# Optimization experiments

Hardware: AMD Instinct MI355X
Metric: run time of the kernel (lower is better)

Reference implementation:

```python
import jax, jax.numpy as jnp
import numpy as np

B, C, H, W = 8, 512, 32, 32
NUM_HEADS = 8
NUM_GROUPS = 32
EPS = 1e-5


def setup_inputs() -> dict:
    key = jax.random.key(0)
    k1, k2, k3 = jax.random.split(key, 3)
    x = jax.random.normal(k1, (B, C, H, W), dtype=jnp.float32)
    gn_w = jnp.ones((C,), dtype=jnp.float32)
    gn_b = jnp.zeros((C,), dtype=jnp.float32)
    qkv_w = jax.random.normal(k2, (3 * C, C), dtype=jnp.float32) * 0.02
    qkv_b = jnp.zeros((3 * C,), dtype=jnp.float32)
    # NOTE: original zero-initializes proj_out; we use random weights so the
    # residual branch is non-trivial for correctness testing.
    proj_w = jax.random.normal(k3, (C, C), dtype=jnp.float32) * 0.02
    proj_b = jnp.zeros((C,), dtype=jnp.float32)
    return {"x": x, "gn_w": gn_w, "gn_b": gn_b, "qkv_w": qkv_w,
            "qkv_b": qkv_b, "proj_w": proj_w, "proj_b": proj_b}


def _group_norm(x, w, b):
    # x: [B, C, T]
    Bn, Cn, T = x.shape
    xg = x.reshape(Bn, NUM_GROUPS, Cn // NUM_GROUPS, T)
    mean = xg.mean(axis=(2, 3), keepdims=True)
    var = xg.var(axis=(2, 3), keepdims=True)
    xn = ((xg - mean) * jax.lax.rsqrt(var + EPS)).reshape(Bn, Cn, T)
    return xn * w[None, :, None] + b[None, :, None]


def reference(x, gn_w, gn_b, qkv_w, qkv_b, proj_w, proj_b):
    b, c = x.shape[0], x.shape[1]
    spatial = x.shape[2:]
    xr = x.reshape(b, c, -1)                      # [B, C, T]
    xn = _group_norm(xr, gn_w, gn_b)
    # 1x1 conv1d: [3C, C] x [B, C, T] -> [B, 3C, T]
    qkv = jnp.einsum('oc,bct->bot', qkv_w, xn) + qkv_b[None, :, None]
    T = qkv.shape[-1]
    qkv = qkv.reshape(b * NUM_HEADS, -1, T)       # [B*Nh, 3*ch, T]
    ch = qkv.shape[1] // 3
    q, k, v = jnp.split(qkv, 3, axis=1)
    scale = 1.0 / np.sqrt(np.sqrt(ch))
    weight = jnp.einsum('bct,bcs->bts', q * scale, k * scale)  # [B*Nh, T, T]
    weight = jax.nn.softmax(weight.astype(jnp.float32), axis=-1).astype(weight.dtype)
    h = jnp.einsum('bts,bcs->bct', weight, v)     # [B*Nh, ch, T]
    h = h.reshape(b, c, T)
    h = jnp.einsum('oc,bct->bot', proj_w, h) + proj_b[None, :, None]
    return (xr + h).reshape(b, c, *spatial)
```

## Files before the change

### kernel.cpp

```cpp
#include <hip/hip_runtime.h>
#include <math.h>

#define Bn 8
#define Cn 512
#define Tn 1024

typedef __attribute__((ext_vector_type(8))) short bf16x8;
typedef __attribute__((ext_vector_type(4))) float f32x4;

__device__ __forceinline__ unsigned short f2bf(float f) {
  unsigned int u = __builtin_bit_cast(unsigned int, f);
  u = (u + 0x7FFFu + ((u >> 16) & 1u)) >> 16;
  return (unsigned short)u;
}

typedef __attribute__((address_space(1))) const unsigned int GU32;
typedef __attribute__((address_space(3))) unsigned int LU32;
__device__ __forceinline__ void gld16(const unsigned short* g, unsigned short* l) {
  __builtin_amdgcn_global_load_lds((GU32*)g, (LU32*)l, 16, 0, 0);
}

__device__ __forceinline__ void stage128x64(const unsigned short* __restrict__ src,
                                            size_t row_stride, unsigned short* lds, int tid) {
  const int w = tid >> 6;
  const int row = tid >> 3;
  const int sc = (tid & 7) ^ ((tid >> 3) & 7);
#pragma unroll
  for (int c = 0; c < 4; ++c)
    gld16(src + (size_t)(c * 32 + row) * row_stride + sc * 8,
          (unsigned short*)((char*)lds + c * 4096 + w * 1024));
}

__device__ __forceinline__ void stage64x64(const unsigned short* __restrict__ src,
                                           size_t row_stride, unsigned short* lds, int tid) {
  const int w = tid >> 6;
  const int row = tid >> 3;
  const int sc = (tid & 7) ^ ((tid >> 3) & 7);
#pragma unroll
  for (int c = 0; c < 2; ++c)
    gld16(src + (size_t)(c * 32 + row) * row_stride + sc * 8,
          (unsigned short*)((char*)lds + c * 4096 + w * 1024));
}

__global__ __launch_bounds__(256) void gn_kernel(const float* __restrict__ x,
                                                 const float* __restrict__ gw,
                                                 const float* __restrict__ gb,
                                                 unsigned short* __restrict__ xn_t) {
  const int blk = blockIdx.x;
  const int b = blk >> 5, g = blk & 31;
  const size_t base = ((size_t)b * Cn + (size_t)g * 16) * Tn;
  const float4* __restrict__ xin = (const float4*)(x + base);
  const int tid = threadIdx.x;

  float vv[16][4];
  float sum = 0.f, sq = 0.f;
#pragma unroll
  for (int k = 0; k < 16; ++k) {
    const float4 t4 = xin[tid + (k << 8)];
    vv[k][0] = t4.x; vv[k][1] = t4.y; vv[k][2] = t4.z; vv[k][3] = t4.w;
    sum += t4.x + t4.y + t4.z + t4.w;
    sq += t4.x * t4.x + t4.y * t4.y + t4.z * t4.z + t4.w * t4.w;
  }

  __shared__ float rs[8];
  const int lane = tid & 63, wv = tid >> 6;
#pragma unroll
  for (int off = 32; off > 0; off >>= 1) {
    sum += __shfl_down(sum, off);
    sq += __shfl_down(sq, off);
  }
  if (lane == 0) { rs[wv] = sum; rs[4 + wv] = sq; }
  __syncthreads();
  const float ts = rs[0] + rs[1] + rs[2] + rs[3];
  const float tq = rs[4] + rs[5] + rs[6] + rs[7];
  const float mean = ts * (1.f / 16384.f);
  const float var = tq * (1.f / 16384.f) - mean * mean;
  const float rstd = rsqrtf(var + 1e-5f);

  float aa[16], bb[16];
#pragma unroll
  for (int k = 0; k < 16; ++k) {
    aa[k] = rstd * gw[g * 16 + k];
    bb[k] = gb[g * 16 + k] - mean * aa[k];
  }

#pragma unroll
  for (int j = 0; j < 4; ++j) {
    const int t = tid * 4 + j;
    unsigned int pk[8];
#pragma unroll
    for (int k2 = 0; k2 < 8; ++k2) {
      const unsigned int lo = f2bf(vv[2 * k2][j] * aa[2 * k2] + bb[2 * k2]);
      const unsigned int hi = f2bf(vv[2 * k2 + 1][j] * aa[2 * k2 + 1] + bb[2 * k2 + 1]);
      pk[k2] = lo | (hi << 16);
    }
    unsigned short* dst = xn_t + ((size_t)(b * Tn + t)) * Cn + g * 16;
    *(uint4*)dst = make_uint4(pk[0], pk[1], pk[2], pk[3]);
    *((uint4*)dst + 1) = make_uint4(pk[4], pk[5], pk[6], pk[7]);
  }
}

__global__ __launch_bounds__(256) void cvt_kernel(const float* __restrict__ src,
                                                  unsigned short* __restrict__ dst, int n4) {
  const int i = blockIdx.x * 256 + threadIdx.x;
  if (i < n4) {
    const float4 f = ((const float4*)src)[i];
    uint2 o;
    o.x = (unsigned int)f2bf(f.x) | ((unsigned int)f2bf(f.y) << 16);
    o.y = (unsigned int)f2bf(f.z) | ((unsigned int)f2bf(f.w) << 16);
    ((uint2*)dst)[i] = o;
  }
}

__global__ __launch_bounds__(256, 2) void qkv_gemm(const unsigned short* __restrict__ Wb,
                                                   const unsigned short* __restrict__ Xb,
                                                   const float* __restrict__ bias,
                                                   unsigned short* __restrict__ q_t,
                                                   unsigned short* __restrict__ k_t,
                                                   unsigned short* __restrict__ v_t) {
  __shared__ unsigned short As[2][8192];
  __shared__ unsigned short Bs[2][8192];
  const int id = blockIdx.x;
  const int b = id & 7;
  const int inner = id >> 3;
  const int bx = inner % 12, by = inner / 12;
  const int o0 = bx * 128, t0 = by * 128;
  const int tid = threadIdx.x, lane = tid & 63, w = tid >> 6;
  const int wr = w >> 1, wc = w & 1;
  const int ln = lane & 15, g16 = lane >> 4;
  const unsigned short* __restrict__ X = Xb + (size_t)b * Tn * Cn;
  const unsigned short* __restrict__ Wt = Wb + (size_t)o0 * 512;
  const unsigned short* __restrict__ Xt = X + (size_t)t0 * 512;

  f32x4 acc[4][4];
#pragma unroll
  for (int mt = 0; mt < 4; ++mt)
#pragma unroll
    for (int nt = 0; nt < 4; ++nt) acc[mt][nt] = (f32x4){0.f, 0.f, 0.f, 0.f};

  stage128x64(Wt, 512, &As[0][0], tid);
  stage128x64(Xt, 512, &Bs[0][0], tid);
  __syncthreads();

  int buf = 0;
  for (int k0 = 0; k0 < 512; k0 += 64) {
    if (k0 + 64 < 512) {
      stage128x64(Wt + k0 + 64, 512, &As[buf ^ 1][0], tid);
      stage128x64(Xt + k0 + 64, 512, &Bs[buf ^ 1][0], tid);
    }
    const char* Ab = (const char*)&As[buf][0];
    const char* Bb = (const char*)&Bs[buf][0];
    bf16x8 af[4][2], bfr[4][2];
#pragma unroll
    for (int mt = 0; mt < 4; ++mt)
#pragma unroll
      for (int kk = 0; kk < 2; ++kk) {
        const int row = wr * 64 + mt * 16 + ln;
        const int c16 = ((kk << 2) | g16) ^ (ln & 7);
        af[mt][kk] = *(const bf16x8*)(Ab + row * 128 + (c16 << 4));
      }
#pragma unroll
    for (int nt = 0; nt < 4; ++nt)
#pragma unroll
      for (int kk = 0; kk < 2; ++kk) {
        const int row = wc * 64 + nt * 16 + ln;
        const int c16 = ((kk << 2) | g16) ^ (ln & 7);
        bfr[nt][kk] = *(const bf16x8*)(Bb + row * 128 + (c16 << 4));
      }
#pragma unroll
    for (int kk = 0; kk < 2; ++kk)
#pragma unroll
      for (int mt = 0; mt < 4; ++mt)
#pragma unroll
        for (int nt = 0; nt < 4; ++nt)
          acc[mt][nt] =
              __builtin_amdgcn_mfma_f32_16x16x32_bf16(af[mt][kk], bfr[nt][kk], acc[mt][nt], 0, 0, 0);
    __syncthreads();
    buf ^= 1;
  }

  const int o_base = o0 + wr * 64, t_base = t0 + wc * 64;
#pragma unroll
  for (int mt = 0; mt < 4; ++mt) {
    const int ob16 = o_base + mt * 16;
    const int part = (ob16 >> 6) % 3;
    const int hh = ob16 / 192;
    const int c16 = ob16 & 63;
    const int bh = b * 8 + hh;
    float bv[4];
#pragma unroll
    for (int r = 0; r < 4; ++r) bv[r] = bias[ob16 + g16 * 4 + r];
#pragma unroll
    for (int nt = 0; nt < 4; ++nt) {
      const int t = t_base + nt * 16 + ln;
      float v0 = acc[mt][nt][0] + bv[0];
      float v1 = acc[mt][nt][1] + bv[1];
      float v2 = acc[mt][nt][2] + bv[2];
      float v3 = acc[mt][nt][3] + bv[3];
      if (part == 0) { v0 *= 0.125f; v1 *= 0.125f; v2 *= 0.125f; v3 *= 0.125f; }
      if (part < 2) {
        unsigned short* dst = (part == 0 ? q_t : k_t) + (size_t)bh * 65536 + (size_t)t * 64 +
                              c16 + g16 * 4;
        uint2 pk;
        pk.x = (unsigned int)f2bf(v0) | ((unsigned int)f2bf(v1) << 16);
        pk.y = (unsigned int)f2bf(v2) | ((unsigned int)f2bf(v3) << 16);
        *(uint2*)dst = pk;
      } else {
        unsigned short* dst = v_t + (size_t)bh * 65536 + (size_t)(c16 + g16 * 4) * Tn + t;
        dst[0] = f2bf(v0);
        dst[1024] = f2bf(v1);
        dst[2048] = f2bf(v2);
        dst[3072] = f2bf(v3);
      }
    }
  }
}

__global__ __launch_bounds__(256, 2) void attn_kernel(const unsigned short* __restrict__ q_t,
                                                      const unsigned short* __restrict__ k_t,
                                                      const unsigned short* __restrict__ v_t,
                                                      unsigned short* __restrict__ h_t) {
  __shared__ unsigned short Ks[2][4096];
  __shared__ unsigned short Vs[2][4096];
  __shared__ unsigned short P_lds[4][32][72];
  const int id = blockIdx.x;
  const int bh = ((id >> 6) << 3) | (id & 7);
  const int tc = (id >> 3) & 7;
  const int tid = threadIdx.x, lane = tid & 63, w = tid >> 6;
  const int t_wave = tc * 128 + w * 32;
  const int ln = lane & 15, g16 = lane >> 4, g8 = g16 * 8;
  const unsigned short* __restrict__ qbase = q_t + (size_t)bh * 65536;
  const unsigned short* __restrict__ kbase = k_t + (size_t)bh * 65536;
  const unsigned short* __restrict__ vbase = v_t + (size_t)bh * 65536;

  bf16x8 qf[2][2];
#pragma unroll
  for (int mt = 0; mt < 2; ++mt)
#pragma unroll
    for (int kb = 0; kb < 2; ++kb)
      qf[mt][kb] = *(const bf16x8*)(qbase + (size_t)(t_wave + mt * 16 + ln) * 64 + kb * 32 + g8);

  f32x4 o_acc[2][4];
  float m_run[2][4], l_run[2][4];
#pragma unroll
  for (int mt = 0; mt < 2; ++mt) {
#pragma unroll
    for (int nc = 0; nc < 4; ++nc) o_acc[mt][nc] = (f32x4){0.f, 0.f, 0.f, 0.f};
#pragma unroll
    for (int r = 0; r < 4; ++r) { m_run[mt][r] = -1e30f; l_run[mt][r] = 0.f; }
  }

  stage64x64(kbase, 64, &Ks[0][0], tid);
  stage64x64(vbase, 1024, &Vs[0][0], tid);
  __syncthreads();

  int buf = 0;
  for (int st = 0; st < 16; ++st) {
    if (st < 15) {
      const int s0n = (st + 1) << 6;
      stage64x64(kbase + (size_t)s0n * 64, 64, &Ks[buf ^ 1][0], tid);
      stage64x64(vbase + s0n, 1024, &Vs[buf ^ 1][0], tid);
    }
    const char* Kb = (const char*)&Ks[buf][0];
    const char* Vb = (const char*)&Vs[buf][0];

    f32x4 sacc[2][4];
#pragma unroll
    for (int mt = 0; mt < 2; ++mt)
#pragma unroll
      for (int ns = 0; ns < 4; ++ns) sacc[mt][ns] = (f32x4){0.f, 0.f, 0.f, 0.f};

#pragma unroll
    for (int ns = 0; ns < 4; ++ns)
#pragma unroll
      for (int kb = 0; kb < 2; ++kb) {
        const int row = ns * 16 + ln;
        const int c16 = ((kb << 2) | g16) ^ (ln & 7);
        const bf16x8 kf = *(const bf16x8*)(Kb + row * 128 + (c16 << 4));
        sacc[0][ns] = __builtin_amdgcn_mfma_f32_16x16x32_bf16(qf[0][kb], kf, sacc[0][ns], 0, 0, 0);
        sacc[1][ns] = __builtin_amdgcn_mfma_f32_16x16x32_bf16(qf[1][kb], kf, sacc[1][ns], 0, 0, 0);
      }

    float mx[2][4];
    bool need = false;
#pragma unroll
    for (int mt = 0; mt < 2; ++mt)
#pragma unroll
      for (int r = 0; r < 4; ++r) {
        float m = fmaxf(fmaxf(sacc[mt][0][r], sacc[mt][1][r]),
                        fmaxf(sacc[mt][2][r], sacc[mt][3][r]));
        m = fmaxf(m, __shfl_xor(m, 1));
        m = fmaxf(m, __shfl_xor(m, 2));
        m = fmaxf(m, __shfl_xor(m, 4));
        m = fmaxf(m, __shfl_xor(m, 8));
        mx[mt][r] = m;
        need = need || (m > m_run[mt][r] + 8.f);
      }
    if (__any(need ? 1 : 0)) {
#pragma unroll
      for (int mt = 0; mt < 2; ++mt)
#pragma unroll
        for (int r = 0; r < 4; ++r) {
          const float mnew = fmaxf(m_run[mt][r], mx[mt][r]);
          const float al = __expf(m_run[mt][r] - mnew);
          m_run[mt][r] = mnew;
          l_run[mt][r] *= al;
#pragma unroll
          for (int nc = 0; nc < 4; ++nc) o_acc[mt][nc][r] *= al;
        }
    }

#pragma unroll
    for (int mt = 0; mt < 2; ++mt)
#pragma unroll
      for (int r = 0; r < 4; ++r) {
        const int trow = mt * 16 + g16 * 4 + r;
        const float mref = m_run[mt][r];
        float rsum = 0.f;
#pragma unroll
        for (int ns = 0; ns < 4; ++ns) {
          const float pv = __expf(sacc[mt][ns][r] - mref);
          rsum += pv;
          P_lds[w][trow][ns * 16 + ln] = f2bf(pv);
        }
        rsum += __shfl_xor(rsum, 1);
        rsum += __shfl_xor(rsum, 2);
        rsum += __shfl_xor(rsum, 4);
        rsum += __shfl_xor(rsum, 8);
        l_run[mt][r] += rsum;
      }

    bf16x8 pf[2][2];
#pragma unroll
    for (int mt = 0; mt < 2; ++mt)
#pragma unroll
      for (int kb = 0; kb < 2; ++kb)
        pf[mt][kb] = *(const bf16x8*)&P_lds[w][mt * 16 + ln][kb * 32 + g8];

#pragma unroll
    for (int kb = 0; kb < 2; ++kb)
#pragma unroll
      for (int nc = 0; nc < 4; ++nc) {
        const int row = nc * 16 + ln;
        const int c16 = ((kb << 2) | g16) ^ (ln & 7);
        const bf16x8 vf = *(const bf16x8*)(Vb + row * 128 + (c16 << 4));
        o_acc[0][nc] = __builtin_amdgcn_mfma_f32_16x16x32_bf16(pf[0][kb], vf, o_acc[0][nc], 0, 0, 0);
        o_acc[1][nc] = __builtin_amdgcn_mfma_f32_16x16x32_bf16(pf[1][kb], vf, o_acc[1][nc], 0, 0, 0);
      }
    __syncthreads();
    buf ^= 1;
  }

  const int b = bh >> 3, hh = bh & 7;
  unsigned short* __restrict__ hb = h_t + (size_t)b * Tn * Cn + hh * 64;
#pragma unroll
  for (int mt = 0; mt < 2; ++mt) {
    float rl[4];
#pragma unroll
    for (int r = 0; r < 4; ++r) rl[r] = 1.f / l_run[mt][r];
#pragma unroll
    for (int nc = 0; nc < 4; ++nc) {
      const int c = nc * 16 + ln;
#pragma unroll
      for (int r = 0; r < 4; ++r) {
        const int t = t_wave + mt * 16 + g16 * 4 + r;
        hb[(size_t)t * Cn + c] = f2bf(o_acc[mt][nc][r] * rl[r]);
      }
    }
  }
}

__global__ __launch_bounds__(256, 2) void proj_gemm(const unsigned short* __restrict__ Wb,
                                                    const unsigned short* __restrict__ Hb,
                                                    const float* __restrict__ pbias,
                                                    const float* __restrict__ x,
                                                    float* __restrict__ out) {
  __shared__ unsigned short As[2][8192];
  __shared__ unsigned short Bs[2][8192];
  const int id = blockIdx.x;
  const int b = id & 7;
  const int inner = id >> 3;
  const int bx = inner & 3, by = inner >> 2;
  const int o0 = bx * 128, t0 = by * 128;
  const int tid = threadIdx.x, lane = tid & 63, w = tid >> 6;
  const int wr = w >> 1, wc = w & 1;
  const int ln = lane & 15, g16 = lane >> 4;
  const unsigned short* __restrict__ H = Hb + (size_t)b * Tn * Cn;
  const unsigned short* __restrict__ Wt = Wb + (size_t)o0 * 512;
  const unsigned short* __restrict__ Ht = H + (size_t)t0 * 512;

  f32x4 acc[4][4];
#pragma unroll
  for (int mt = 0; mt < 4; ++mt)
#pragma unroll
    for (int nt = 0; nt < 4; ++nt) acc[mt][nt] = (f32x4){0.f, 0.f, 0.f, 0.f};

  stage128x64(Wt, 512, &As[0][0], tid);
  stage128x64(Ht, 512, &Bs[0][0], tid);
  __syncthreads();

  int buf = 0;
  for (int k0 = 0; k0 < 512; k0 += 64) {
    if (k0 + 64 < 512) {
      stage128x64(Wt + k0 + 64, 512, &As[buf ^ 1][0], tid);
      stage128x64(Ht + k0 + 64, 512, &Bs[buf ^ 1][0], tid);
    }
    const char* Ab = (const char*)&As[buf][0];
    const char* Bb = (const char*)&Bs[buf][0];
    bf16x8 af[4][2], bfr[4][2];
#pragma unroll
    for (int mt = 0; mt < 4; ++mt)
#pragma unroll
      for (int kk = 0; kk < 2; ++kk) {
        const int row = wr * 64 + mt * 16 + ln;
        const int c16 = ((kk << 2) | g16) ^ (ln & 7);
        af[mt][kk] = *(const bf16x8*)(Ab + row * 128 + (c16 << 4));
      }
#pragma unroll
    for (int nt = 0; nt < 4; ++nt)
#pragma unroll
      for (int kk = 0; kk < 2; ++kk) {
        const int row = wc * 64 + nt * 16 + ln;
        const int c16 = ((kk << 2) | g16) ^ (ln & 7);
        bfr[nt][kk] = *(const bf16x8*)(Bb + row * 128 + (c16 << 4));
      }
#pragma unroll
    for (int kk = 0; kk < 2; ++kk)
#pragma unroll
      for (int mt = 0; mt < 4; ++mt)
#pragma unroll
        for (int nt = 0; nt < 4; ++nt)
          acc[mt][nt] =
              __builtin_amdgcn_mfma_f32_16x16x32_bf16(af[mt][kk], bfr[nt][kk], acc[mt][nt], 0, 0, 0);
    __syncthreads();
    buf ^= 1;
  }

  const int o_base = o0 + wr * 64, t_base = t0 + wc * 64;
#pragma unroll
  for (int mt = 0; mt < 4; ++mt) {
    const int ob = o_base + mt * 16 + g16 * 4;
    float pb[4];
#pragma unroll
    for (int r = 0; r < 4; ++r) pb[r] = pbias[ob + r];
#pragma unroll
    for (int nt = 0; nt < 4; ++nt) {
      const int t = t_base + nt * 16 + ln;
#pragma unroll
      for (int r = 0; r < 4; ++r) {
        const size_t idx = (size_t)b * Cn * Tn + (size_t)(ob + r) * Tn + t;
        out[idx] = acc[mt][nt][r] + pb[r] + x[idx];
      }
    }
  }
}

extern "C" void kernel_launch(void* const* d_in, const int* in_sizes, int n_in,
                              void* d_out, int out_size, void* d_ws, size_t ws_size,
                              hipStream_t stream) {
  (void)in_sizes; (void)n_in; (void)out_size; (void)ws_size;
  const float* x = (const float*)d_in[0];
  const float* gn_w = (const float*)d_in[1];
  const float* gn_b = (const float*)d_in[2];
  const float* qkv_w = (const float*)d_in[3];
  const float* qkv_b = (const float*)d_in[4];
  const float* proj_w = (const float*)d_in[5];
  const float* proj_b = (const float*)d_in[6];
  float* out = (float*)d_out;

  unsigned short* wsu = (unsigned short*)d_ws;
  unsigned short* xn_t = wsu;
  unsigned short* wqkv = xn_t + (size_t)4194304;
  unsigned short* wproj = wqkv + (size_t)786432;
  unsigned short* q_t = wproj + (size_t)262144;
  unsigned short* k_t = q_t + (size_t)4194304;
  unsigned short* v_t = k_t + (size_t)4194304;
  unsigned short* h_t = v_t + (size_t)4194304;

  gn_kernel<<<dim3(256), 256, 0, stream>>>(x, gn_w, gn_b, xn_t);
  cvt_kernel<<<dim3(768), 256, 0, stream>>>(qkv_w, wqkv, 196608);
  cvt_kernel<<<dim3(256), 256, 0, stream>>>(proj_w, wproj, 65536);
  qkv_gemm<<<dim3(768), 256, 0, stream>>>(wqkv, xn_t, qkv_b, q_t, k_t, v_t);
  attn_kernel<<<dim3(512), 256, 0, stream>>>(q_t, k_t, v_t, h_t);
  proj_gemm<<<dim3(256), 256, 0, stream>>>(wproj, h_t, proj_b, x, out);
}
```

Baseline: 181.3 us.

## Stage V transpose through LDS in QKV GEMM and load K/V directly in attention

The QKV GEMM epilogue now writes V tiles into LDS and then emits coalesced 16-byte stores to the transposed V buffer, replacing scattered 2-byte stores. The attention kernel drops its LDS double-buffered K/V staging and barriers. It loads K and V fragments straight from global memory into registers, prefetching the next K tile, and wraps the MFMA blocks in s_setprio. It also switches to 128-thread blocks over twice as many workgroups. This relies on the cache to absorb repeated K/V reads across waves and gives up explicit LDS sharing between waves.

```diff
diff --git a/kernel.cpp b/kernel.cpp
--- a/kernel.cpp
+++ b/kernel.cpp
@@ -27,17 +27,6 @@
   const int sc = (tid & 7) ^ ((tid >> 3) & 7);
 #pragma unroll
   for (int c = 0; c < 4; ++c)
-    gld16(src + (size_t)(c * 32 + row) * row_stride + sc * 8,
-          (unsigned short*)((char*)lds + c * 4096 + w * 1024));
-}
-
-__device__ __forceinline__ void stage64x64(const unsigned short* __restrict__ src,
-                                           size_t row_stride, unsigned short* lds, int tid) {
-  const int w = tid >> 6;
-  const int row = tid >> 3;
-  const int sc = (tid & 7) ^ ((tid >> 3) & 7);
-#pragma unroll
-  for (int c = 0; c < 2; ++c)
     gld16(src + (size_t)(c * 32 + row) * row_stride + sc * 8,
           (unsigned short*)((char*)lds + c * 4096 + w * 1024));
 }
@@ -180,54 +169,74 @@
   }
 
   const int o_base = o0 + wr * 64, t_base = t0 + wc * 64;
-#pragma unroll
-  for (int mt = 0; mt < 4; ++mt) {
-    const int ob16 = o_base + mt * 16;
-    const int part = (ob16 >> 6) % 3;
-    const int hh = ob16 / 192;
-    const int c16 = ob16 & 63;
-    const int bh = b * 8 + hh;
-    float bv[4];
-#pragma unroll
-    for (int r = 0; r < 4; ++r) bv[r] = bias[ob16 + g16 * 4 + r];
-#pragma unroll
-    for (int nt = 0; nt < 4; ++nt) {
-      const int t = t_base + nt * 16 + ln;
-      float v0 = acc[mt][nt][0] + bv[0];
-      float v1 = acc[mt][nt][1] + bv[1];
-      float v2 = acc[mt][nt][2] + bv[2];
-      float v3 = acc[mt][nt][3] + bv[3];
-      if (part == 0) { v0 *= 0.125f; v1 *= 0.125f; v2 *= 0.125f; v3 *= 0.125f; }
-      if (part < 2) {
-        unsigned short* dst = (part == 0 ? q_t : k_t) + (size_t)bh * 65536 + (size_t)t * 64 +
-                              c16 + g16 * 4;
+  const int partw = (o_base >> 6) % 3;
+  const int bh = b * 8 + o_base / 192;
+  unsigned short (*Vlds)[136] = (unsigned short (*)[136])(&As[0][0]);
+
+  if (partw < 2) {
+    unsigned short* qk = (partw == 0 ? q_t : k_t) + (size_t)bh * 65536;
+    const float sc = (partw == 0) ? 0.125f : 1.0f;
+#pragma unroll
+    for (int mt = 0; mt < 4; ++mt) {
+      const int ob16 = o_base + mt * 16;
+      float bv[4];
+#pragma unroll
+      for (int r = 0; r < 4; ++r) bv[r] = bias[ob16 + g16 * 4 + r];
+#pragma unroll
+      for (int nt = 0; nt < 4; ++nt) {
+        const int t = t_base + nt * 16 + ln;
+        const float v0 = (acc[mt][nt][0] + bv[0]) * sc;
+        const float v1 = (acc[mt][nt][1] + bv[1]) * sc;
+        const float v2 = (acc[mt][nt][2] + bv[2]) * sc;
+        const float v3 = (acc[mt][nt][3] + bv[3]) * sc;
         uint2 pk;
         pk.x = (unsigned int)f2bf(v0) | ((unsigned int)f2bf(v1) << 16);
         pk.y = (unsigned int)f2bf(v2) | ((unsigned int)f2bf(v3) << 16);
-        *(uint2*)dst = pk;
-      } else {
-        unsigned short* dst = v_t + (size_t)bh * 65536 + (size_t)(c16 + g16 * 4) * Tn + t;
-        dst[0] = f2bf(v0);
-        dst[1024] = f2bf(v1);
-        dst[2048] = f2bf(v2);
-        dst[3072] = f2bf(v3);
-      }
-    }
-  }
-}
-
-__global__ __launch_bounds__(256, 2) void attn_kernel(const unsigned short* __restrict__ q_t,
+        *(uint2*)(qk + (size_t)t * 64 + mt * 16 + g16 * 4) = pk;
+      }
+    }
+  } else {
+#pragma unroll
+    for (int mt = 0; mt < 4; ++mt) {
+      float bv[4];
+#pragma unroll
+      for (int r = 0; r < 4; ++r) bv[r] = bias[o_base + mt * 16 + g16 * 4 + r];
+#pragma unroll
+      for (int nt = 0; nt < 4; ++nt)
+#pragma unroll
+        for (int r = 0; r < 4; ++r)
+          Vlds[mt * 16 + g16 * 4 + r][wc * 64 + nt * 16 + ln] = f2bf(acc[mt][nt][r] + bv[r]);
+    }
+  }
+  __syncthreads();
+  const int bxm = bx % 3;
+  if (bxm) {
+    const int o_first = o0 + (bxm - 1) * 64;
+    unsigned short* vdst = v_t + (size_t)(b * 8 + o_first / 192) * 65536;
+    const int c = tid >> 2, tseg = (tid & 3) << 5;
+    const unsigned short* src = &Vlds[c][tseg];
+    unsigned short* p = vdst + (size_t)c * Tn + t0 + tseg;
+    const uint4 d0 = *(const uint4*)(src);
+    const uint4 d1 = *(const uint4*)(src + 8);
+    const uint4 d2 = *(const uint4*)(src + 16);
+    const uint4 d3 = *(const uint4*)(src + 24);
+    *(uint4*)(p) = d0;
+    *(uint4*)(p + 8) = d1;
+    *(uint4*)(p + 16) = d2;
+    *(uint4*)(p + 24) = d3;
+  }
+}
+
+__global__ __launch_bounds__(128, 2) void attn_kernel(const unsigned short* __restrict__ q_t,
                                                       const unsigned short* __restrict__ k_t,
                                                       const unsigned short* __restrict__ v_t,
                                                       unsigned short* __restrict__ h_t) {
-  __shared__ unsigned short Ks[2][4096];
-  __shared__ unsigned short Vs[2][4096];
-  __shared__ unsigned short P_lds[4][32][72];
+  __shared__ unsigned short P_lds[2][32][72];
   const int id = blockIdx.x;
-  const int bh = ((id >> 6) << 3) | (id & 7);
-  const int tc = (id >> 3) & 7;
+  const int bh = ((id >> 7) << 3) | (id & 7);
+  const int tc = (id >> 3) & 15;
   const int tid = threadIdx.x, lane = tid & 63, w = tid >> 6;
-  const int t_wave = tc * 128 + w * 32;
+  const int t_wave = tc * 64 + w * 32;
   const int ln = lane & 15, g16 = lane >> 4, g8 = g16 * 8;
   const unsigned short* __restrict__ qbase = q_t + (size_t)bh * 65536;
   const unsigned short* __restrict__ kbase = k_t + (size_t)bh * 65536;
@@ -250,36 +259,37 @@
     for (int r = 0; r < 4; ++r) { m_run[mt][r] = -1e30f; l_run[mt][r] = 0.f; }
   }
 
-  stage64x64(kbase, 64, &Ks[0][0], tid);
-  stage64x64(vbase, 1024, &Vs[0][0], tid);
-  __syncthreads();
-
-  int buf = 0;
+  bf16x8 kf[4][2];
+#pragma unroll
+  for (int ns = 0; ns < 4; ++ns)
+#pragma unroll
+    for (int kb = 0; kb < 2; ++kb)
+      kf[ns][kb] = *(const bf16x8*)(kbase + (size_t)(ns * 16 + ln) * 64 + kb * 32 + g8);
+
   for (int st = 0; st < 16; ++st) {
-    if (st < 15) {
-      const int s0n = (st + 1) << 6;
-      stage64x64(kbase + (size_t)s0n * 64, 64, &Ks[buf ^ 1][0], tid);
-      stage64x64(vbase + s0n, 1024, &Vs[buf ^ 1][0], tid);
-    }
-    const char* Kb = (const char*)&Ks[buf][0];
-    const char* Vb = (const char*)&Vs[buf][0];
-
+    const int s0 = st << 6;
     f32x4 sacc[2][4];
 #pragma unroll
     for (int mt = 0; mt < 2; ++mt)
 #pragma unroll
       for (int ns = 0; ns < 4; ++ns) sacc[mt][ns] = (f32x4){0.f, 0.f, 0.f, 0.f};
 
+    __builtin_amdgcn_s_setprio(1);
 #pragma unroll
     for (int ns = 0; ns < 4; ++ns)
 #pragma unroll
       for (int kb = 0; kb < 2; ++kb) {
-        const int row = ns * 16 + ln;
-        const int c16 = ((kb << 2) | g16) ^ (ln & 7);
-        const bf16x8 kf = *(const bf16x8*)(Kb + row * 128 + (c16 << 4));
-        sacc[0][ns] = __builtin_amdgcn_mfma_f32_16x16x32_bf16(qf[0][kb], kf, sacc[0][ns], 0, 0, 0);
-        sacc[1][ns] = __builtin_amdgcn_mfma_f32_16x16x32_bf16(qf[1][kb], kf, sacc[1][ns], 0, 0, 0);
-      }
+        sacc[0][ns] = __builtin_amdgcn_mfma_f32_16x16x32_bf16(qf[0][kb], kf[ns][kb], sacc[0][ns], 0, 0, 0);
+        sacc[1][ns] = __builtin_amdgcn_mfma_f32_16x16x32_bf16(qf[1][kb], kf[ns][kb], sacc[1][ns], 0, 0, 0);
+      }
+    __builtin_amdgcn_s_setprio(0);
+
+    bf16x8 vf[4][2];
+#pragma unroll
+    for (int nc = 0; nc < 4; ++nc)
+#pragma unroll
+      for (int kb = 0; kb < 2; ++kb)
+        vf[nc][kb] = *(const bf16x8*)(vbase + (size_t)(nc * 16 + ln) * Tn + s0 + kb * 32 + g8);
 
     float mx[2][4];
     bool need = false;
@@ -330,6 +340,15 @@
         l_run[mt][r] += rsum;
       }
 
+    if (st < 15) {
+#pragma unroll
+      for (int ns = 0; ns < 4; ++ns)
+#pragma unroll
+        for (int kb = 0; kb < 2; ++kb)
+          kf[ns][kb] =
+              *(const bf16x8*)(kbase + (size_t)(s0 + 64 + ns * 16 + ln) * 64 + kb * 32 + g8);
+    }
+
     bf16x8 pf[2][2];
 #pragma unroll
     for (int mt = 0; mt < 2; ++mt)
@@ -337,18 +356,15 @@
       for (int kb = 0; kb < 2; ++kb)
         pf[mt][kb] = *(const bf16x8*)&P_lds[w][mt * 16 + ln][kb * 32 + g8];
 
+    __builtin_amdgcn_s_setprio(1);
 #pragma unroll
     for (int kb = 0; kb < 2; ++kb)
 #pragma unroll
       for (int nc = 0; nc < 4; ++nc) {
-        const int row = nc * 16 + ln;
-        const int c16 = ((kb << 2) | g16) ^ (ln & 7);
-        const bf16x8 vf = *(const bf16x8*)(Vb + row * 128 + (c16 << 4));
-        o_acc[0][nc] = __builtin_amdgcn_mfma_f32_16x16x32_bf16(pf[0][kb], vf, o_acc[0][nc], 0, 0, 0);
-        o_acc[1][nc] = __builtin_amdgcn_mfma_f32_16x16x32_bf16(pf[1][kb], vf, o_acc[1][nc], 0, 0, 0);
-      }
-    __syncthreads();
-    buf ^= 1;
+        o_acc[0][nc] = __builtin_amdgcn_mfma_f32_16x16x32_bf16(pf[0][kb], vf[nc][kb], o_acc[0][nc], 0, 0, 0);
+        o_acc[1][nc] = __builtin_amdgcn_mfma_f32_16x16x32_bf16(pf[1][kb], vf[nc][kb], o_acc[1][nc], 0, 0, 0);
+      }
+    __builtin_amdgcn_s_setprio(0);
   }
 
   const int b = bh >> 3, hh = bh & 7;
@@ -481,6 +497,6 @@
   cvt_kernel<<<dim3(768), 256, 0, stream>>>(qkv_w, wqkv, 196608);
   cvt_kernel<<<dim3(256), 256, 0, stream>>>(proj_w, wproj, 65536);
   qkv_gemm<<<dim3(768), 256, 0, stream>>>(wqkv, xn_t, qkv_b, q_t, k_t, v_t);
-  attn_kernel<<<dim3(512), 256, 0, stream>>>(q_t, k_t, v_t, h_t);
+  attn_kernel<<<dim3(1024), 128, 0, stream>>>(q_t, k_t, v_t, h_t);
   proj_gemm<<<dim3(256), 256, 0, stream>>>(wproj, h_t, proj_b, x, out);
 }
```

New measurement: 188.2 us. 3.8% more time.
